# Kernel tuning notes

Hardware: AMD Instinct MI355X
Metric: run time of the kernel (lower is better)

The kernel has to match this reference:

```python
import jax, jax.numpy as jnp
import numpy as np

N = 100000      # nodes
E = 1600000     # edges (avg degree 16)
IN_DIM = 16
D = 128         # layer width
H = 2           # attention heads (GATLayer default n_heads=2)
FC = 128
OUT_DIM = 4
L = 2           # len(layer_channels)-1 attention layers


def _gat_layer(x, src, dst, Wk, bk, Wq, bq, Wv, bv):
    # x: [N, D]; src/dst: [E]
    n = x.shape[0]
    dk = D // H
    k = (x @ Wk + bk).reshape(n, H, dk)
    q = (x @ Wq + bq).reshape(n, H, dk)
    v = (x @ Wv + bv).reshape(n, H, dk)
    # per-edge score: k_src . q_dst  -> [E, H]
    score = jnp.einsum('ehd,ehd->eh', k[src], q[dst])
    # edge softmax grouped by destination node
    smax = jax.ops.segment_max(score, dst, num_segments=n)          # [N, H]
    ex = jnp.exp(score - smax[dst])                                 # [E, H]
    denom = jax.ops.segment_sum(ex, dst, num_segments=n)           # [N, H]
    attn = ex / denom[dst]                                          # [E, H]
    # weighted scatter-sum of source values to destinations
    msg = v[src] * attn[:, :, None]                                 # [E, H, dk]
    res = jax.ops.segment_sum(msg, dst, num_segments=n)             # [N, H, dk]
    return res.reshape(n, D)


def setup_inputs() -> dict:
    key = jax.random.key(0)
    ks = jax.random.split(key, 24)
    def lin(k, fin, fout):
        w = jax.random.normal(k, (fin, fout), jnp.float32) * (1.0 / np.sqrt(fin))
        return w
    inp = {}
    inp['x'] = jax.random.normal(ks[0], (N, IN_DIM), jnp.float32)
    inp['src'] = jax.random.randint(ks[1], (E,), 0, N, jnp.int32)
    inp['dst'] = jax.random.randint(ks[2], (E,), 0, N, jnp.int32)
    inp['fc0_w'] = lin(ks[3], IN_DIM, D)
    inp['fc0_b'] = jnp.zeros((D,), jnp.float32)
    inp['Wk'] = jnp.stack([lin(ks[4 + i], D, D) for i in range(L)])
    inp['bk'] = jnp.zeros((L, D), jnp.float32)
    inp['Wq'] = jnp.stack([lin(ks[6 + i], D, D) for i in range(L)])
    inp['bq'] = jnp.zeros((L, D), jnp.float32)
    inp['Wv'] = jnp.stack([lin(ks[8 + i], D, D) for i in range(L)])
    inp['bv'] = jnp.zeros((L, D), jnp.float32)
    inp['ws_w'] = jnp.stack([lin(ks[10 + i], D, D) for i in range(L)])
    inp['ws_b'] = jnp.zeros((L, D), jnp.float32)
    inp['fc1_w'] = lin(ks[12], D, FC)
    inp['fc1_b'] = jnp.zeros((FC,), jnp.float32)
    inp['fc2_w'] = lin(ks[13], FC, OUT_DIM)
    inp['fc2_b'] = jnp.zeros((OUT_DIM,), jnp.float32)
    return inp


def reference(x, src, dst, fc0_w, fc0_b, Wk, bk, Wq, bq, Wv, bv, ws_w, ws_b, fc1_w, fc1_b, fc2_w, fc2_b):
    h = x @ fc0_w + fc0_b                                           # [N, D]
    for i in range(L):
        h = (h @ ws_w[i] + ws_b[i]) + _gat_layer(h, src, dst, Wk[i], bk[i], Wq[i], bq[i], Wv[i], bv[i])
        if i != L - 1:
            h = jax.nn.gelu(h)
    h = jax.nn.gelu(h @ fc1_w + fc1_b)                              # fc_channels > 0 branch
    return h @ fc2_w + fc2_b                                        # [N, OUT_DIM]
```

## Files before the change

### kernel.cpp

```cpp
#include <hip/hip_runtime.h>
#include <math.h>


typedef _Float16 f16x8 __attribute__((ext_vector_type(8)));
typedef _Float16 h2 __attribute__((ext_vector_type(2)));
typedef float f32x4 __attribute__((ext_vector_type(4)));

__device__ __forceinline__ ushort f2h(float x) {
    union { _Float16 h; ushort u; } v;
    v.h = (_Float16)x;
    return v.u;
}
__device__ __forceinline__ float h2f(ushort u) {
    union { ushort u; _Float16 h; } v;
    v.u = u;
    return (float)v.h;
}

__device__ __forceinline__ float gelu_f(float x) {
    float y = 0.7978845608028654f * (x + 0.044715f * x * x * x);
    float t = __expf(2.f * y);
    return x * t / (t + 1.f);
}

__device__ __forceinline__ h2 pk2(float a, float b) {
    return __builtin_bit_cast(h2, __builtin_amdgcn_cvt_pkrtz(a, b));
}

__global__ void k_zero(int* __restrict__ p, int n) {
    int i = blockIdx.x * blockDim.x + threadIdx.x;
    if (i < n) p[i] = 0;
}

__global__ void k_hist(const int* __restrict__ dst, int* __restrict__ deg,
                       int* __restrict__ rank, int e) {
    int i = blockIdx.x * blockDim.x + threadIdx.x;
    if (i < e) rank[i] = atomicAdd(&deg[dst[i]], 1);
}

__global__ __launch_bounds__(256) void k_part(const int* __restrict__ deg,
                                              int* __restrict__ pre,
                                              int* __restrict__ bsum, int n) {
    __shared__ int lds[256];
    int t = threadIdx.x;
    int base = blockIdx.x * 1024 + t * 4;
    int d0 = 0, d1 = 0, d2 = 0, d3 = 0;
    if (base + 3 < n) {
        int4 d = *(const int4*)&deg[base];
        d0 = d.x; d1 = d.y; d2 = d.z; d3 = d.w;
    } else {
        if (base + 0 < n) d0 = deg[base + 0];
        if (base + 1 < n) d1 = deg[base + 1];
        if (base + 2 < n) d2 = deg[base + 2];
        if (base + 3 < n) d3 = deg[base + 3];
    }
    int s0 = d0, s1 = s0 + d1, s2 = s1 + d2, s3 = s2 + d3;
    lds[t] = s3;
    __syncthreads();
    for (int off = 1; off < 256; off <<= 1) {
        int v = (t >= off) ? lds[t - off] : 0;
        __syncthreads();
        lds[t] += v;
        __syncthreads();
    }
    int excl = lds[t] - s3;
    if (base + 0 < n) pre[base + 0] = excl;
    if (base + 1 < n) pre[base + 1] = excl + s0;
    if (base + 2 < n) pre[base + 2] = excl + s1;
    if (base + 3 < n) pre[base + 3] = excl + s2;
    if (t == 255) bsum[blockIdx.x] = lds[255];
}

__global__ void k_scanb(int* __restrict__ bsum, int nb) {
    __shared__ int lds[128];
    int t = threadIdx.x;
    int v = (t < nb) ? bsum[t] : 0;
    lds[t] = v;
    __syncthreads();
    for (int off = 1; off < 128; off <<= 1) {
        int u = (t >= off) ? lds[t - off] : 0;
        __syncthreads();
        lds[t] += u;
        __syncthreads();
    }
    if (t < nb) bsum[t] = lds[t] - v;
}

__global__ __launch_bounds__(256) void k_add(int* __restrict__ rowp,
                                             const int* __restrict__ bsum, int n,
                                             int e) {
    int t = threadIdx.x;
    int base = blockIdx.x * 1024 + t * 4;
    int off = bsum[blockIdx.x];
#pragma unroll
    for (int j = 0; j < 4; ++j) {
        int i = base + j;
        if (i < n) rowp[i] += off;
    }
    if (blockIdx.x == 0 && t == 0) rowp[n] = e;
}

__global__ void k_scatter(const int* __restrict__ src, const int* __restrict__ dst,
                          const int* __restrict__ rank, const int* __restrict__ rowp,
                          int* __restrict__ csrc, int e) {
    int i = blockIdx.x * blockDim.x + threadIdx.x;
    if (i < e) csrc[rowp[dst[i]] + rank[i]] = src[i];
}

__global__ void k_pack(const float* __restrict__ Wk, const float* __restrict__ Wq,
                       const float* __restrict__ Wv, const float* __restrict__ Ws,
                       const float* __restrict__ Wfc1, ushort* __restrict__ Wp) {
    int id = blockIdx.y;
    const float* src;
    if (id < 8) {
        int m = id & 3, layer = id >> 2;
        src = (m == 0) ? Wk : (m == 1) ? Wq : (m == 2) ? Wv : Ws;
        src += layer * 16384;
    } else {
        src = Wfc1;
    }
    int o = blockIdx.x * 256 + threadIdx.x;
    int j = o & 7, l = (o >> 3) & 63, nf = (o >> 9) & 7, kc = o >> 12;
    int row = kc * 32 + ((l >> 4) << 3) + j;
    int col = nf * 16 + (l & 15);
    Wp[id * 16384 + o] = f2h(src[row * 128 + col]);
}

__global__ __launch_bounds__(256) void k_fc0(const float* __restrict__ X,
                                             const float* __restrict__ W,
                                             const float* __restrict__ b,
                                             ushort* __restrict__ H, int n) {
    __shared__ float Ws[16 * 128];
    __shared__ float xs[2][16];
    int t = threadIdx.x;
#pragma unroll
    for (int i = 0; i < 8; ++i) Ws[t + i * 256] = W[t + i * 256];
    if (t < 32) {
        int nn = blockIdx.x * 2 + (t >> 4);
        xs[t >> 4][t & 15] = (nn < n) ? X[nn * 16 + (t & 15)] : 0.f;
    }
    __syncthreads();
    int nd = blockIdx.x * 2 + (t >> 7);
    if (nd < n) {
        int c = t & 127;
        float acc = b[c];
#pragma unroll
        for (int j = 0; j < 16; ++j) acc += xs[t >> 7][j] * Ws[j * 128 + c];
        H[(size_t)nd * 128 + c] = f2h(acc);
    }
}

__device__ __forceinline__ void stage_Ah(const ushort* __restrict__ A, int n,
                                         int rbase, char* Asb, int t) {
#pragma unroll
    for (int i = 0; i < 4; ++i) {
        int b = t * 16 + i * 4096;
        int r = b >> 8;
        uint4 v = {0u, 0u, 0u, 0u};
        if (rbase + r < n)
            v = *(const uint4*)((const char*)A + (size_t)rbase * 256 + b);
        *(uint4*)(Asb + (b ^ ((r & 7) << 4))) = v;
    }
}

__global__ __launch_bounds__(256) void k_gemm_proj(
    const ushort* __restrict__ A, int n, const ushort* __restrict__ Wp,
    const float* __restrict__ b0, ushort* __restrict__ o0,
    const float* __restrict__ b1, ushort* __restrict__ o1,
    const float* __restrict__ b2_, ushort* __restrict__ o2,
    const float* __restrict__ b3, ushort* __restrict__ o3) {
    __shared__ ushort As[64 * 128];
    __shared__ ushort Ws[16384];
    char* Asb = (char*)As;
    int t = threadIdx.x;
    int rbase = blockIdx.x * 64;

    stage_Ah(A, n, rbase, Asb, t);

    const uint4* wsrc = (const uint4*)Wp;
    uint4 wreg[8];
#pragma unroll
    for (int i = 0; i < 8; ++i) wreg[i] = wsrc[t + i * 256];

    __syncthreads();

    int w = t >> 6, l = t & 63;
    int arow = w * 16 + (l & 15);
    int kq = l >> 4;

    f16x8 a[4];
#pragma unroll
    for (int kc = 0; kc < 4; ++kc) {
        int byte = (arow * 256 + kc * 64 + kq * 16) ^ ((arow & 7) << 4);
        a[kc] = *(const f16x8*)(Asb + byte);
    }
    __syncthreads();

    for (int m = 0; m < 4; ++m) {
#pragma unroll
        for (int i = 0; i < 8; ++i) ((uint4*)Ws)[t + i * 256] = wreg[i];
        __syncthreads();

        if (m < 3) {
#pragma unroll
            for (int i = 0; i < 8; ++i)
                wreg[i] = wsrc[(m + 1) * 2048 + t + i * 256];
        }

        const float* bias; ushort* op;
        if (m == 0)      { bias = b0; op = o0; }
        else if (m == 1) { bias = b1; op = o1; }
        else if (m == 2) { bias = b2_; op = o2; }
        else             { bias = b3; op = o3; }

        f32x4 acc[8];
#pragma unroll
        for (int nf = 0; nf < 8; ++nf) acc[nf] = (f32x4){0.f, 0.f, 0.f, 0.f};

#pragma unroll
        for (int kc = 0; kc < 4; ++kc) {
#pragma unroll
            for (int nf = 0; nf < 8; ++nf) {
                f16x8 b = *(const f16x8*)(Ws + (((kc * 8 + nf) * 64 + l) << 3));
                acc[nf] = __builtin_amdgcn_mfma_f32_16x16x32_f16(a[kc], b, acc[nf], 0, 0, 0);
            }
        }
        __syncthreads();

#pragma unroll
        for (int nf = 0; nf < 8; ++nf) {
            int col = nf * 16 + (l & 15);
            float bia = bias[col];
#pragma unroll
            for (int r = 0; r < 4; ++r) {
                int row = w * 16 + (l >> 4) * 4 + r;
                int b = (row * 256 + col * 2) ^ ((row & 7) << 4);
                *(ushort*)(Asb + b) = f2h(acc[nf][r] + bia);
            }
        }
        __syncthreads();

#pragma unroll
        for (int i = 0; i < 4; ++i) {
            int b = t * 16 + i * 4096;
            int r = b >> 8;
            uint4 v = *(const uint4*)(Asb + (b ^ ((r & 7) << 4)));
            if (rbase + r < n)
                *(uint4*)((char*)op + (size_t)rbase * 256 + b) = v;
        }
    }
}

__global__ __launch_bounds__(256) void k_gemm_fc(
    const ushort* __restrict__ A, int n, const ushort* __restrict__ Wp,
    const float* __restrict__ bias1, const float* __restrict__ W2,
    const float* __restrict__ bias2, float* __restrict__ out2) {
    __shared__ ushort As[64 * 128];
    __shared__ ushort Ws[16384];
    char* Asb = (char*)As;
    int t = threadIdx.x;
    int rbase = blockIdx.x * 64;

    stage_Ah(A, n, rbase, Asb, t);

    const uint4* wsrc = (const uint4*)Wp;
#pragma unroll
    for (int i = 0; i < 8; ++i) ((uint4*)Ws)[t + i * 256] = wsrc[t + i * 256];

    __syncthreads();

    int w = t >> 6, l = t & 63;
    int arow = w * 16 + (l & 15);
    int kq = l >> 4;

    f16x8 a[4];
#pragma unroll
    for (int kc = 0; kc < 4; ++kc) {
        int byte = (arow * 256 + kc * 64 + kq * 16) ^ ((arow & 7) << 4);
        a[kc] = *(const f16x8*)(Asb + byte);
    }

    f32x4 acc[8];
#pragma unroll
    for (int nf = 0; nf < 8; ++nf) acc[nf] = (f32x4){0.f, 0.f, 0.f, 0.f};

#pragma unroll
    for (int kc = 0; kc < 4; ++kc) {
#pragma unroll
        for (int nf = 0; nf < 8; ++nf) {
            f16x8 b = *(const f16x8*)(Ws + (((kc * 8 + nf) * 64 + l) << 3));
            acc[nf] = __builtin_amdgcn_mfma_f32_16x16x32_f16(a[kc], b, acc[nf], 0, 0, 0);
        }
    }

    float pj[4][4];
#pragma unroll
    for (int r = 0; r < 4; ++r)
#pragma unroll
        for (int j = 0; j < 4; ++j) pj[r][j] = 0.f;
#pragma unroll
    for (int nf = 0; nf < 8; ++nf) {
        int col = nf * 16 + (l & 15);
        float4 w2v = *(const float4*)&W2[col * 4];
        float bia = bias1[col];
#pragma unroll
        for (int r = 0; r < 4; ++r) {
            float o = gelu_f(acc[nf][r] + bia);
            pj[r][0] += o * w2v.x;
            pj[r][1] += o * w2v.y;
            pj[r][2] += o * w2v.z;
            pj[r][3] += o * w2v.w;
        }
    }
#pragma unroll
    for (int off = 1; off < 16; off <<= 1)
#pragma unroll
        for (int r = 0; r < 4; ++r)
#pragma unroll
            for (int j = 0; j < 4; ++j)
                pj[r][j] += __shfl_xor(pj[r][j], off);
    int jj = l & 15;
    if (jj < 4) {
#pragma unroll
        for (int r = 0; r < 4; ++r) {
            int row = rbase + w * 16 + (l >> 4) * 4 + r;
            if (row < n) {
                float v = (jj == 0) ? pj[r][0] : (jj == 1) ? pj[r][1]
                        : (jj == 2) ? pj[r][2] : pj[r][3];
                out2[(size_t)row * 4 + jj] = v + bias2[jj];
            }
        }
    }
}

__global__ void k_edge_hf(const ushort* __restrict__ K, const ushort* __restrict__ Q,
                          const ushort* __restrict__ V, const int* __restrict__ rowp,
                          const int* __restrict__ csrc, ushort* __restrict__ H, int n,
                          int act) {
    int wid = (int)((blockIdx.x * blockDim.x + threadIdx.x) >> 6);
    int lane = threadIdx.x & 63;
    if (wid >= n) return;
    int qb = lane >> 4;
    unsigned fb = (lane & 15) * 8u;
    int e0 = rowp[wid], e1 = rowp[wid + 1];

    uint4 qr = *(const uint4*)(Q + (((unsigned)wid << 7) + fb));
    h2 q0 = __builtin_bit_cast(h2, qr.x), q1 = __builtin_bit_cast(h2, qr.y);
    h2 q2 = __builtin_bit_cast(h2, qr.z), q3 = __builtin_bit_cast(h2, qr.w);

    float m = -1e30f, denom = 0.f;
    h2 hz = {(_Float16)0.f, (_Float16)0.f};
    h2 acc0 = hz, acc1 = hz, acc2 = hz, acc3 = hz;

    for (int eb = e0; eb < e1; eb += 64) {
        int cnt = min(64, e1 - eb);
        int sl = (eb + lane < e1) ? csrc[eb + lane] : 0;
        int full = cnt >> 2;
#pragma unroll 2
        for (int j = 0; j < full; ++j) {
            int s = __shfl(sl, 4 * j + qb);
            unsigned off = ((unsigned)s << 7) + fb;
            uint4 kr = *(const uint4*)(K + off);
            float sc = __builtin_amdgcn_fdot2(__builtin_bit_cast(h2, kr.x), q0,
                       __builtin_amdgcn_fdot2(__builtin_bit_cast(h2, kr.y), q1,
                       __builtin_amdgcn_fdot2(__builtin_bit_cast(h2, kr.z), q2,
                       __builtin_amdgcn_fdot2(__builtin_bit_cast(h2, kr.w), q3,
                                              0.f, false), false), false), false);
            sc += __shfl_xor(sc, 1);
            sc += __shfl_xor(sc, 2);
            sc += __shfl_xor(sc, 4);
            uint4 vr = *(const uint4*)(V + off);
            float mn = fmaxf(m, sc);
            float ss = __expf(m - mn);
            float p = __expf(sc - mn);
            denom = denom * ss + p;
            h2 hp = pk2(p, p);
            h2 hs = pk2(ss, ss);
            acc0 = __builtin_bit_cast(h2, vr.x) * hp + acc0 * hs;
            acc1 = __builtin_bit_cast(h2, vr.y) * hp + acc1 * hs;
            acc2 = __builtin_bit_cast(h2, vr.z) * hp + acc2 * hs;
            acc3 = __builtin_bit_cast(h2, vr.w) * hp + acc3 * hs;
            m = mn;
        }
        int rem = cnt & 3;
        if (rem) {
            bool val = qb < rem;
            int s = __shfl(sl, full * 4 + qb);
            unsigned off = ((unsigned)s << 7) + fb;
            uint4 kr = *(const uint4*)(K + off);
            float sc = __builtin_amdgcn_fdot2(__builtin_bit_cast(h2, kr.x), q0,
                       __builtin_amdgcn_fdot2(__builtin_bit_cast(h2, kr.y), q1,
                       __builtin_amdgcn_fdot2(__builtin_bit_cast(h2, kr.z), q2,
                       __builtin_amdgcn_fdot2(__builtin_bit_cast(h2, kr.w), q3,
                                              0.f, false), false), false), false);
            sc += __shfl_xor(sc, 1);
            sc += __shfl_xor(sc, 2);
            sc += __shfl_xor(sc, 4);
            uint4 vr = *(const uint4*)(V + off);
            float mn = val ? fmaxf(m, sc) : m;
            float ss = __expf(m - mn);
            float p = val ? __expf(sc - mn) : 0.f;
            denom = denom * ss + p;
            h2 hp = pk2(p, p);
            h2 hs = pk2(ss, ss);
            acc0 = __builtin_bit_cast(h2, vr.x) * hp + acc0 * hs;
            acc1 = __builtin_bit_cast(h2, vr.y) * hp + acc1 * hs;
            acc2 = __builtin_bit_cast(h2, vr.z) * hp + acc2 * hs;
            acc3 = __builtin_bit_cast(h2, vr.w) * hp + acc3 * hs;
            m = mn;
        }
    }

#pragma unroll
    for (int dist = 16; dist <= 32; dist <<= 1) {
        float mo = __shfl_xor(m, dist);
        float dn = __shfl_xor(denom, dist);
        unsigned w0 = __shfl_xor(__builtin_bit_cast(unsigned, acc0), dist);
        unsigned w1 = __shfl_xor(__builtin_bit_cast(unsigned, acc1), dist);
        unsigned w2 = __shfl_xor(__builtin_bit_cast(unsigned, acc2), dist);
        unsigned w3 = __shfl_xor(__builtin_bit_cast(unsigned, acc3), dist);
        float mn = fmaxf(m, mo);
        float sA = __expf(m - mn), sB = __expf(mo - mn);
        denom = denom * sA + dn * sB;
        h2 hA = pk2(sA, sA), hB = pk2(sB, sB);
        acc0 = acc0 * hA + __builtin_bit_cast(h2, w0) * hB;
        acc1 = acc1 * hA + __builtin_bit_cast(h2, w1) * hB;
        acc2 = acc2 * hA + __builtin_bit_cast(h2, w2) * hB;
        acc3 = acc3 * hA + __builtin_bit_cast(h2, w3) * hB;
        m = mn;
    }

    if (lane < 16) {
        float inv = (denom > 0.f) ? 1.f / denom : 0.f;
        ushort* hp = H + (((unsigned)wid << 7) + fb);
        uint4 hr = *(const uint4*)hp;
        h2 s0 = __builtin_bit_cast(h2, hr.x), s1 = __builtin_bit_cast(h2, hr.y);
        h2 s2 = __builtin_bit_cast(h2, hr.z), s3 = __builtin_bit_cast(h2, hr.w);
        float o0 = (float)s0.x + (float)acc0.x * inv;
        float o1 = (float)s0.y + (float)acc0.y * inv;
        float o2 = (float)s1.x + (float)acc1.x * inv;
        float o3 = (float)s1.y + (float)acc1.y * inv;
        float o4 = (float)s2.x + (float)acc2.x * inv;
        float o5 = (float)s2.y + (float)acc2.y * inv;
        float o6 = (float)s3.x + (float)acc3.x * inv;
        float o7 = (float)s3.y + (float)acc3.y * inv;
        if (act) {
            o0 = gelu_f(o0); o1 = gelu_f(o1); o2 = gelu_f(o2); o3 = gelu_f(o3);
            o4 = gelu_f(o4); o5 = gelu_f(o5); o6 = gelu_f(o6); o7 = gelu_f(o7);
        }
        uint4 o;
        o.x = __builtin_bit_cast(unsigned, pk2(o0, o1));
        o.y = __builtin_bit_cast(unsigned, pk2(o2, o3));
        o.z = __builtin_bit_cast(unsigned, pk2(o4, o5));
        o.w = __builtin_bit_cast(unsigned, pk2(o6, o7));
        *(uint4*)hp = o;
    }
}

extern "C" void kernel_launch(void* const* d_in, const int* in_sizes, int n_in,
                              void* d_out, int out_size, void* d_ws, size_t ws_size,
                              hipStream_t stream) {
    const float* x     = (const float*)d_in[0];
    const int*   src   = (const int*)d_in[1];
    const int*   dst   = (const int*)d_in[2];
    const float* fc0_w = (const float*)d_in[3];
    const float* fc0_b = (const float*)d_in[4];
    const float* Wk    = (const float*)d_in[5];
    const float* bk    = (const float*)d_in[6];
    const float* Wq    = (const float*)d_in[7];
    const float* bq    = (const float*)d_in[8];
    const float* Wv    = (const float*)d_in[9];
    const float* bv    = (const float*)d_in[10];
    const float* ws_w  = (const float*)d_in[11];
    const float* ws_b  = (const float*)d_in[12];
    const float* fc1_w = (const float*)d_in[13];
    const float* fc1_b = (const float*)d_in[14];
    const float* fc2_w = (const float*)d_in[15];
    const float* fc2_b = (const float*)d_in[16];

    int n = in_sizes[0] / 16;
    int e = in_sizes[1];

    ushort* hA  = (ushort*)d_ws;
    ushort* hB  = hA + (size_t)n * 128;
    ushort* Kb  = hB + (size_t)n * 128;
    ushort* Qb  = Kb + (size_t)n * 128;
    ushort* Vb  = Qb + (size_t)n * 128;
    ushort* Wp  = Vb + (size_t)n * 128;
    int* deg    = (int*)(Wp + 9 * 16384);
    int* rowp   = deg + n;
    int* csrc   = rowp + n + 1;
    int* rank   = csrc + e;
    int* bsum   = rank + e;

    int nb = (n + 1023) / 1024;

    k_zero<<<(n + 255) / 256, 256, 0, stream>>>(deg, n);
    k_hist<<<(e + 255) / 256, 256, 0, stream>>>(dst, deg, rank, e);
    k_part<<<nb, 256, 0, stream>>>(deg, rowp, bsum, n);
    k_scanb<<<1, 128, 0, stream>>>(bsum, nb);
    k_add<<<nb, 256, 0, stream>>>(rowp, bsum, n, e);
    k_scatter<<<(e + 255) / 256, 256, 0, stream>>>(src, dst, rank, rowp, csrc, e);

    k_pack<<<dim3(64, 9), 256, 0, stream>>>(Wk, Wq, Wv, ws_w, fc1_w, Wp);

    k_fc0<<<(n + 1) / 2, 256, 0, stream>>>(x, fc0_w, fc0_b, hA, n);

    int gx = (n + 63) / 64;
    k_gemm_proj<<<gx, 256, 0, stream>>>(hA, n, Wp, bk, Kb, bq, Qb, bv, Vb, ws_b, hB);
    k_edge_hf<<<(n + 3) / 4, 256, 0, stream>>>(Kb, Qb, Vb, rowp, csrc, hB, n, 1);
    k_gemm_proj<<<gx, 256, 0, stream>>>(hB, n, Wp + 4 * 16384, bk + 128, Kb,
                                        bq + 128, Qb, bv + 128, Vb, ws_b + 128, hA);
    k_edge_hf<<<(n + 3) / 4, 256, 0, stream>>>(Kb, Qb, Vb, rowp, csrc, hA, n, 0);

    k_gemm_fc<<<gx, 256, 0, stream>>>(hA, n, Wp + 8 * 16384, fc1_b, fc2_w, fc2_b,
                                      (float*)d_out);
}
```

Baseline: 544.7 us.

## Interleave K and V rows and use lazy max rescaling in edge softmax

K and V projections are now written into one interleaved buffer with a 256-element row stride, so each gathered source node's key and value sit in the same 512-byte span and share cache lines and DRAM pages. The online softmax in the edge kernel now rescales the accumulators only when a score exceeds the running max by more than 4. This removes the per-edge exps and accumulator multiplies. The lazy threshold lets unnormalized fp16 accumulators grow by up to about e^4 before rescaling, which slightly raises overflow and precision risk.

After: 545.6 us. No clear change (+0.2%).

```diff
diff --git a/kernel.cpp b/kernel.cpp
--- a/kernel.cpp
+++ b/kernel.cpp
@@ -10,11 +10,6 @@
     union { _Float16 h; ushort u; } v;
     v.h = (_Float16)x;
     return v.u;
-}
-__device__ __forceinline__ float h2f(ushort u) {
-    union { ushort u; _Float16 h; } v;
-    v.u = u;
-    return (float)v.h;
 }
 
 __device__ __forceinline__ float gelu_f(float x) {
@@ -165,10 +160,10 @@
 
 __global__ __launch_bounds__(256) void k_gemm_proj(
     const ushort* __restrict__ A, int n, const ushort* __restrict__ Wp,
-    const float* __restrict__ b0, ushort* __restrict__ o0,
-    const float* __restrict__ b1, ushort* __restrict__ o1,
-    const float* __restrict__ b2_, ushort* __restrict__ o2,
-    const float* __restrict__ b3, ushort* __restrict__ o3) {
+    const float* __restrict__ b0, ushort* __restrict__ o0, int ostr0,
+    const float* __restrict__ b1, ushort* __restrict__ o1, int ostr1,
+    const float* __restrict__ b2_, ushort* __restrict__ o2, int ostr2,
+    const float* __restrict__ b3, ushort* __restrict__ o3, int ostr3) {
     __shared__ ushort As[64 * 128];
     __shared__ ushort Ws[16384];
     char* Asb = (char*)As;
@@ -207,11 +202,11 @@
                 wreg[i] = wsrc[(m + 1) * 2048 + t + i * 256];
         }
 
-        const float* bias; ushort* op;
-        if (m == 0)      { bias = b0; op = o0; }
-        else if (m == 1) { bias = b1; op = o1; }
-        else if (m == 2) { bias = b2_; op = o2; }
-        else             { bias = b3; op = o3; }
+        const float* bias; ushort* op; int ostr;
+        if (m == 0)      { bias = b0; op = o0; ostr = ostr0; }
+        else if (m == 1) { bias = b1; op = o1; ostr = ostr1; }
+        else if (m == 2) { bias = b2_; op = o2; ostr = ostr2; }
+        else             { bias = b3; op = o3; ostr = ostr3; }
 
         f32x4 acc[8];
 #pragma unroll
@@ -243,10 +238,10 @@
 #pragma unroll
         for (int i = 0; i < 4; ++i) {
             int b = t * 16 + i * 4096;
-            int r = b >> 8;
+            int r = b >> 8, c = b & 255;
             uint4 v = *(const uint4*)(Asb + (b ^ ((r & 7) << 4)));
             if (rbase + r < n)
-                *(uint4*)((char*)op + (size_t)rbase * 256 + b) = v;
+                *(uint4*)((char*)op + (size_t)(rbase + r) * ostr * 2 + c) = v;
         }
     }
 }
@@ -333,10 +328,9 @@
     }
 }
 
-__global__ void k_edge_hf(const ushort* __restrict__ K, const ushort* __restrict__ Q,
-                          const ushort* __restrict__ V, const int* __restrict__ rowp,
-                          const int* __restrict__ csrc, ushort* __restrict__ H, int n,
-                          int act) {
+__global__ void k_edge_hf(const ushort* __restrict__ KV, const ushort* __restrict__ Q,
+                          const int* __restrict__ rowp, const int* __restrict__ csrc,
+                          ushort* __restrict__ H, int n, int act) {
     int wid = (int)((blockIdx.x * blockDim.x + threadIdx.x) >> 6);
     int lane = threadIdx.x & 63;
     if (wid >= n) return;
@@ -359,8 +353,8 @@
 #pragma unroll 2
         for (int j = 0; j < full; ++j) {
             int s = __shfl(sl, 4 * j + qb);
-            unsigned off = ((unsigned)s << 7) + fb;
-            uint4 kr = *(const uint4*)(K + off);
+            unsigned off = ((unsigned)s << 8) + fb;
+            uint4 kr = *(const uint4*)(KV + off);
             float sc = __builtin_amdgcn_fdot2(__builtin_bit_cast(h2, kr.x), q0,
                        __builtin_amdgcn_fdot2(__builtin_bit_cast(h2, kr.y), q1,
                        __builtin_amdgcn_fdot2(__builtin_bit_cast(h2, kr.z), q2,
@@ -369,25 +363,28 @@
             sc += __shfl_xor(sc, 1);
             sc += __shfl_xor(sc, 2);
             sc += __shfl_xor(sc, 4);
-            uint4 vr = *(const uint4*)(V + off);
-            float mn = fmaxf(m, sc);
-            float ss = __expf(m - mn);
-            float p = __expf(sc - mn);
-            denom = denom * ss + p;
+            uint4 vr = *(const uint4*)(KV + off + 128);
+            if (sc > m + 4.f) {
+                float ss = __expf(m - sc);
+                m = sc;
+                denom *= ss;
+                h2 hs = pk2(ss, ss);
+                acc0 *= hs; acc1 *= hs; acc2 *= hs; acc3 *= hs;
+            }
+            float p = __expf(sc - m);
+            denom += p;
             h2 hp = pk2(p, p);
-            h2 hs = pk2(ss, ss);
-            acc0 = __builtin_bit_cast(h2, vr.x) * hp + acc0 * hs;
-            acc1 = __builtin_bit_cast(h2, vr.y) * hp + acc1 * hs;
-            acc2 = __builtin_bit_cast(h2, vr.z) * hp + acc2 * hs;
-            acc3 = __builtin_bit_cast(h2, vr.w) * hp + acc3 * hs;
-            m = mn;
+            acc0 = __builtin_bit_cast(h2, vr.x) * hp + acc0;
+            acc1 = __builtin_bit_cast(h2, vr.y) * hp + acc1;
+            acc2 = __builtin_bit_cast(h2, vr.z) * hp + acc2;
+            acc3 = __builtin_bit_cast(h2, vr.w) * hp + acc3;
         }
         int rem = cnt & 3;
         if (rem) {
             bool val = qb < rem;
             int s = __shfl(sl, full * 4 + qb);
-            unsigned off = ((unsigned)s << 7) + fb;
-            uint4 kr = *(const uint4*)(K + off);
+            unsigned off = ((unsigned)s << 8) + fb;
+            uint4 kr = *(const uint4*)(KV + off);
             float sc = __builtin_amdgcn_fdot2(__builtin_bit_cast(h2, kr.x), q0,
                        __builtin_amdgcn_fdot2(__builtin_bit_cast(h2, kr.y), q1,
                        __builtin_amdgcn_fdot2(__builtin_bit_cast(h2, kr.z), q2,
@@ -396,18 +393,21 @@
             sc += __shfl_xor(sc, 1);
             sc += __shfl_xor(sc, 2);
             sc += __shfl_xor(sc, 4);
-            uint4 vr = *(const uint4*)(V + off);
-            float mn = val ? fmaxf(m, sc) : m;
-            float ss = __expf(m - mn);
-            float p = val ? __expf(sc - mn) : 0.f;
-            denom = denom * ss + p;
+            uint4 vr = *(const uint4*)(KV + off + 128);
+            if (val && sc > m + 4.f) {
+                float ss = __expf(m - sc);
+                m = sc;
+                denom *= ss;
+                h2 hs = pk2(ss, ss);
+                acc0 *= hs; acc1 *= hs; acc2 *= hs; acc3 *= hs;
+            }
+            float p = val ? __expf(sc - m) : 0.f;
+            denom += p;
             h2 hp = pk2(p, p);
-            h2 hs = pk2(ss, ss);
-            acc0 = __builtin_bit_cast(h2, vr.x) * hp + acc0 * hs;
-            acc1 = __builtin_bit_cast(h2, vr.y) * hp + acc1 * hs;
-            acc2 = __builtin_bit_cast(h2, vr.z) * hp + acc2 * hs;
-            acc3 = __builtin_bit_cast(h2, vr.w) * hp + acc3 * hs;
-            m = mn;
+            acc0 = __builtin_bit_cast(h2, vr.x) * hp + acc0;
+            acc1 = __builtin_bit_cast(h2, vr.y) * hp + acc1;
+            acc2 = __builtin_bit_cast(h2, vr.z) * hp + acc2;
+            acc3 = __builtin_bit_cast(h2, vr.w) * hp + acc3;
         }
     }
 
@@ -483,10 +483,9 @@
 
     ushort* hA  = (ushort*)d_ws;
     ushort* hB  = hA + (size_t)n * 128;
-    ushort* Kb  = hB + (size_t)n * 128;
-    ushort* Qb  = Kb + (size_t)n * 128;
-    ushort* Vb  = Qb + (size_t)n * 128;
-    ushort* Wp  = Vb + (size_t)n * 128;
+    ushort* KV  = hB + (size_t)n * 128;
+    ushort* Qb  = KV + (size_t)n * 256;
+    ushort* Wp  = Qb + (size_t)n * 128;
     int* deg    = (int*)(Wp + 9 * 16384);
     int* rowp   = deg + n;
     int* csrc   = rowp + n + 1;
@@ -507,11 +506,13 @@
     k_fc0<<<(n + 1) / 2, 256, 0, stream>>>(x, fc0_w, fc0_b, hA, n);
 
     int gx = (n + 63) / 64;
-    k_gemm_proj<<<gx, 256, 0, stream>>>(hA, n, Wp, bk, Kb, bq, Qb, bv, Vb, ws_b, hB);
-    k_edge_hf<<<(n + 3) / 4, 256, 0, stream>>>(Kb, Qb, Vb, rowp, csrc, hB, n, 1);
-    k_gemm_proj<<<gx, 256, 0, stream>>>(hB, n, Wp + 4 * 16384, bk + 128, Kb,
-                                        bq + 128, Qb, bv + 128, Vb, ws_b + 128, hA);
-    k_edge_hf<<<(n + 3) / 4, 256, 0, stream>>>(Kb, Qb, Vb, rowp, csrc, hA, n, 0);
+    k_gemm_proj<<<gx, 256, 0, stream>>>(hA, n, Wp, bk, KV, 256, bq, Qb, 128,
+                                        bv, KV + 128, 256, ws_b, hB, 128);
+    k_edge_hf<<<(n + 3) / 4, 256, 0, stream>>>(KV, Qb, rowp, csrc, hB, n, 1);
+    k_gemm_proj<<<gx, 256, 0, stream>>>(hB, n, Wp + 4 * 16384, bk + 128, KV, 256,
+                                        bq + 128, Qb, 128, bv + 128, KV + 128, 256,
+                                        ws_b + 128, hA, 128);
+    k_edge_hf<<<(n + 3) / 4, 256, 0, stream>>>(KV, Qb, rowp, csrc, hA, n, 0);
 
     k_gemm_fc<<<gx, 256, 0, stream>>>(hA, n, Wp + 8 * 16384, fc1_b, fc2_w, fc2_b,
                                       (float*)d_out);
```
